# Kernel optimization log

Measured on AMD Instinct MI355X. Metric: run time of the kernel, lower is better.

The kernel has to match this reference:

```python
import jax, jax.numpy as jnp
import numpy as np
from jax import lax

B, T, BYTE_LEN, EMB = 8, 4096, 8, 64
FILTERS = [(1, 4), (2, 8), (3, 12), (4, 16), (5, 20), (6, 24), (7, 28)]
LAST_DIM = sum(c for _, c in FILTERS)  # 112
OUT_DIM = 512


def setup_inputs() -> dict:
    key = jax.random.key(0)
    ks = jax.random.split(key, 32)
    inp = {"features": jax.random.normal(ks[0], (B, T, BYTE_LEN, EMB), dtype=jnp.float32)}
    for i, (w, c) in enumerate(FILTERS):
        inp[f"conv_w{i+1}"] = jax.random.normal(ks[1 + i], (c, EMB, w), dtype=jnp.float32) * 0.05
        inp[f"conv_b{i+1}"] = jax.random.normal(ks[8 + i], (c,), dtype=jnp.float32) * 0.05
    inp["hw_w1"] = jax.random.normal(ks[15], (2 * LAST_DIM, LAST_DIM), dtype=jnp.float32) * 0.05
    inp["hw_b1"] = jnp.concatenate([jnp.zeros(LAST_DIM), jnp.ones(LAST_DIM)]).astype(jnp.float32)
    inp["hw_w2"] = jax.random.normal(ks[16], (2 * LAST_DIM, LAST_DIM), dtype=jnp.float32) * 0.05
    inp["hw_b2"] = jnp.concatenate([jnp.zeros(LAST_DIM), jnp.ones(LAST_DIM)]).astype(jnp.float32)
    inp["proj_w"] = jax.random.normal(ks[17], (OUT_DIM, LAST_DIM), dtype=jnp.float32) * 0.05
    inp["proj_b"] = jax.random.normal(ks[18], (OUT_DIM,), dtype=jnp.float32) * 0.05
    return inp


def _conv_branch(x, w, b):
    # x: [N, EMB, BYTE_LEN], w: [out_c, EMB, width] -> max over time, relu -> [N, out_c]
    y = lax.conv_general_dilated(x, w, window_strides=(1,), padding='VALID',
                                 dimension_numbers=('NCH', 'OIH', 'NCH'))
    y = y + b[None, :, None]
    return jax.nn.relu(jnp.max(y, axis=-1))


def _highway_layer(x, w, b):
    p = x @ w.T + b
    proj_x, gate = jnp.split(p, 2, axis=-1)
    g = jax.nn.sigmoid(gate)
    return g * x + (1.0 - g) * jax.nn.relu(proj_x)


def reference(features, conv_w1, conv_w2, conv_w3, conv_w4, conv_w5, conv_w6, conv_w7,
              conv_b1, conv_b2, conv_b3, conv_b4, conv_b5, conv_b6, conv_b7,
              hw_w1, hw_b1, hw_w2, hw_b2, proj_w, proj_b):
    b, t, byte_len, emb = features.shape
    # transpose(2,3).view(-1, emb, byte_len)
    x = features.transpose(0, 1, 3, 2).reshape(-1, emb, byte_len)  # [B*T, EMB, BYTE_LEN]
    ws = [conv_w1, conv_w2, conv_w3, conv_w4, conv_w5, conv_w6, conv_w7]
    bs = [conv_b1, conv_b2, conv_b3, conv_b4, conv_b5, conv_b6, conv_b7]
    branches = [_conv_branch(x, w, bb) for w, bb in zip(ws, bs)]
    h = jnp.concatenate(branches, axis=-1)  # [B*T, LAST_DIM]
    h = _highway_layer(h, hw_w1, hw_b1)
    h = _highway_layer(h, hw_w2, hw_b2)
    out = h @ proj_w.T + proj_b  # [B*T, OUT_DIM]
    return out.reshape(b, t, -1)
```

## Files before the change

kernel.cpp:

```cpp
#include <hip/hip_runtime.h>

typedef __attribute__((ext_vector_type(8))) short short8;
typedef __attribute__((ext_vector_type(4))) float f32x4;

#define NPOS 32768
#define KDIM 512
#define NCT  30
#define CHUNK_BYTES 30720

__device__ __forceinline__ unsigned short f2bf(float x) {
    unsigned u = __float_as_uint(x);
    return (unsigned short)((u + 0x7FFFu + ((u >> 16) & 1u)) >> 16);
}
__device__ __forceinline__ float bf2f(unsigned short h) {
    return __uint_as_float(((unsigned)h) << 16);
}

__device__ __forceinline__ void stage16(const void* g, void* l, int lane) {
    __builtin_amdgcn_global_load_lds(
        (const __attribute__((address_space(1))) unsigned int*)g,
        (__attribute__((address_space(3))) unsigned int*)l, 16, 0, 0);
}

__global__ void prep_kernel(const float* __restrict__ w1, const float* __restrict__ w2,
                            const float* __restrict__ w3, const float* __restrict__ w4,
                            const float* __restrict__ w5, const float* __restrict__ w6,
                            const float* __restrict__ w7, const float* __restrict__ hw1,
                            const float* __restrict__ hw2, const float* __restrict__ pw,
                            unsigned short* __restrict__ WC, unsigned short* __restrict__ W1s,
                            unsigned short* __restrict__ W2s, unsigned short* __restrict__ Ps) {
    int gid = blockIdx.x * 256 + threadIdx.x;
    if (gid < 245760) {
        int k = gid / 480, col = gid % 480;
        const float* wp; int cbnd, NP, C, W;
        if (col < 32)       { wp = w1; cbnd = 0;   NP = 8; C = 4;  W = 1; }
        else if (col < 96)  { wp = w2; cbnd = 32;  NP = 7; C = 8;  W = 2; }
        else if (col < 176) { wp = w3; cbnd = 96;  NP = 6; C = 12; W = 3; }
        else if (col < 256) { wp = w4; cbnd = 176; NP = 5; C = 16; W = 4; }
        else if (col < 336) { wp = w5; cbnd = 256; NP = 4; C = 20; W = 5; }
        else if (col < 416) { wp = w6; cbnd = 336; NP = 3; C = 24; W = 6; }
        else                { wp = w7; cbnd = 416; NP = 2; C = 28; W = 7; }
        int c2 = col - cbnd, oc = c2 / NP, p = c2 - oc * NP;
        int j = k >> 6, e = k & 63, dk = j - p;
        float v = 0.f;
        if (oc < C && dk >= 0 && dk < W) v = wp[(oc * 64 + e) * W + dk];
        int q = k >> 5, kr = k & 31;
        WC[((q * NCT + (col >> 4)) * 64 + ((kr >> 3) * 16 + (col & 15))) * 8 + (kr & 7)] = f2bf(v);
    } else if (gid < 245760 + 57344) {
        int x = gid - 245760;
        const float* src = (x < 28672) ? hw1 : hw2;
        unsigned short* dst = (x < 28672) ? W1s : W2s;
        if (x >= 28672) x -= 28672;
        int k = x / 224, n = x % 224;
        float v = (k < 112) ? src[n * 112 + k] : 0.f;
        int q = k >> 5, kr = k & 31;
        dst[((q * 14 + (n >> 4)) * 64 + ((kr >> 3) * 16 + (n & 15))) * 8 + (kr & 7)] = f2bf(v);
    } else if (gid < 245760 + 57344 + 65536) {
        int x = gid - 303104;
        int k = x / 512, n = x % 512;
        float v = (k < 112) ? pw[n * 112 + k] : 0.f;
        int q = k >> 5, kr = k & 31;
        Ps[((q * 32 + (n >> 4)) * 64 + ((kr >> 3) * 16 + (n & 15))) * 8 + (kr & 7)] = f2bf(v);
    }
}

template <int T0, int NT>
__device__ __forceinline__ void dump_phase(float* Cb, const f32x4* acc, int wave, int lane) {
    int r0 = wave * 16 + ((lane >> 4) * 4);
    int c0 = lane & 15;
#pragma unroll
    for (int tt = 0; tt < NT; ++tt)
#pragma unroll
        for (int r = 0; r < 4; ++r)
            Cb[(r0 + r) * 161 + tt * 16 + c0] = acc[T0 + tt][r];
}

__device__ void reduce_phase(const float* Cb, unsigned short* ht, int tid,
                             int cA, int NPA, int choffA, int colbA, const float* cbA,
                             int cB, int NPB, int choffB, int colbB, const float* cbB) {
    int noc = cA + cB;
    for (int idx = tid; idx < 64 * noc; idx += 256) {
        int row = idx & 63, ocp = idx >> 6;
        bool isB = ocp >= cA;
        int oc = isB ? ocp - cA : ocp;
        int NP = isB ? NPB : NPA;
        int colb = isB ? colbB : colbA;
        int choff = isB ? choffB : choffA;
        const float* cb = isB ? cbB : cbA;
        const float* src = Cb + row * 161 + colb + oc * NP;
        float m = src[0];
        for (int k = 1; k < NP; ++k) m = fmaxf(m, src[k]);
        float v = fmaxf(m + cb[oc], 0.f);
        ht[row * 128 + choff + oc] = f2bf(v);
    }
}

__global__ __launch_bounds__(256, 2) void conv_gemm(
        const float* __restrict__ feat, const unsigned short* __restrict__ WC,
        const float* cb0, const float* cb1, const float* cb2, const float* cb3,
        const float* cb4, const float* cb5, const float* cb6,
        unsigned short* __restrict__ hg) {
    __shared__ __align__(16) char sm[61440];
    const int tid = threadIdx.x, lane = tid & 63, wave = tid >> 6;
    const int c0 = lane & 15, kq = lane >> 4;
    const int m0 = blockIdx.x * 64;

    const float* arow = feat + (size_t)(m0 + wave * 16 + c0) * KDIM + kq * 8;
    short8 af[16];
#pragma unroll
    for (int q = 0; q < 16; ++q) {
        float t[8];
        *(float4*)(t)     = *(const float4*)(arow + q * 32);
        *(float4*)(t + 4) = *(const float4*)(arow + q * 32 + 4);
        short8 v;
#pragma unroll
        for (int i = 0; i < 8; ++i) v[i] = (short)f2bf(t[i]);
        af[q] = v;
    }

    f32x4 zero = {0.f, 0.f, 0.f, 0.f};
    f32x4 acc[NCT];
#pragma unroll
    for (int t = 0; t < NCT; ++t) acc[t] = zero;

    for (int i = tid; i < 1920; i += 256)
        stage16(WC + i * 8, sm + (i - lane) * 16, lane);

#pragma unroll
    for (int q = 0; q < 16; ++q) {
        __syncthreads();
        if (q < 15) {
            const unsigned short* src = WC + (q + 1) * (CHUNK_BYTES / 2);
            char* dst = sm + ((q + 1) & 1) * CHUNK_BYTES;
            for (int i = tid; i < 1920; i += 256)
                stage16(src + i * 8, dst + (i - lane) * 16, lane);
        }
        const char* bb = sm + (q & 1) * CHUNK_BYTES;
#pragma unroll
        for (int t = 0; t < NCT; ++t) {
            short8 b = *(const short8*)(bb + (t * 64 + lane) * 16);
            acc[t] = __builtin_amdgcn_mfma_f32_16x16x32_bf16(af[q], b, acc[t], 0, 0, 0);
        }
    }

    float* Cb = (float*)sm;
    unsigned short* ht = (unsigned short*)(sm + 41216);
    __syncthreads();
    for (int i = tid; i < 1024; i += 256)
        ht[(i >> 4) * 128 + 112 + (i & 15)] = 0;
    dump_phase<0, 6>(Cb, acc, wave, lane);
    __syncthreads();
    reduce_phase(Cb, ht, tid, 4, 8, 0, 0, cb0, 8, 7, 4, 32, cb1);
    __syncthreads();
    dump_phase<6, 10>(Cb, acc, wave, lane);
    __syncthreads();
    reduce_phase(Cb, ht, tid, 12, 6, 12, 0, cb2, 16, 5, 24, 80, cb3);
    __syncthreads();
    dump_phase<16, 10>(Cb, acc, wave, lane);
    __syncthreads();
    reduce_phase(Cb, ht, tid, 20, 4, 40, 0, cb4, 24, 3, 60, 80, cb5);
    __syncthreads();
    dump_phase<26, 4>(Cb, acc, wave, lane);
    __syncthreads();
    reduce_phase(Cb, ht, tid, 28, 2, 84, 0, cb6, 0, 1, 0, 0, cb6);
    __syncthreads();
    uint4* dst = (uint4*)(hg + (size_t)m0 * 128);
    for (int i = tid; i < 1024; i += 256) dst[i] = ((const uint4*)ht)[i];
}

__global__ __launch_bounds__(256, 2) void tail_kernel(
        const unsigned short* __restrict__ hg, const unsigned short* __restrict__ W1,
        const unsigned short* __restrict__ W2, const unsigned short* __restrict__ PW,
        const float* __restrict__ hb1, const float* __restrict__ hb2,
        const float* __restrict__ pb, float* __restrict__ out) {
    __shared__ __align__(16) char sm[65536];
    const int tid = threadIdx.x, lane = tid & 63, wave = tid >> 6;
    const int c0 = lane & 15, kq = lane >> 4;
    const int m0 = blockIdx.x * 64;
    f32x4 zero = {0.f, 0.f, 0.f, 0.f};

    short8 a2[4];
#pragma unroll
    for (int q = 0; q < 4; ++q)
        a2[q] = *(const short8*)(hg + (size_t)(m0 + wave * 16 + c0) * 128 + q * 32 + kq * 8);

    for (int i = tid; i < 3584; i += 256)
        stage16(W1 + i * 8, sm + (i - lane) * 16, lane);
    __syncthreads();
    f32x4 acc2[14];
#pragma unroll
    for (int t = 0; t < 14; ++t) acc2[t] = zero;
#pragma unroll
    for (int t = 0; t < 14; ++t)
#pragma unroll
        for (int q = 0; q < 4; ++q) {
            short8 b = *(const short8*)(sm + ((q * 14 + t) * 64 + lane) * 16);
            acc2[t] = __builtin_amdgcn_mfma_f32_16x16x32_bf16(a2[q], b, acc2[t], 0, 0, 0);
        }
    __syncthreads();

    unsigned short* ht = (unsigned short*)sm;
#pragma unroll
    for (int t = 0; t < 7; ++t) {
        float bp = hb1[t * 16 + c0], bg = hb1[112 + t * 16 + c0];
#pragma unroll
        for (int r = 0; r < 4; ++r) {
            int row = wave * 16 + kq * 4 + r;
            int col = t * 16 + c0;
            float px = acc2[t][r] + bp;
            float gt = acc2[t + 7][r] + bg;
            float g = 1.f / (1.f + __expf(-gt));
            float hres = bf2f(hg[(size_t)(m0 + row) * 128 + col]);
            ht[row * 136 + col] = f2bf(g * hres + (1.f - g) * fmaxf(px, 0.f));
        }
    }
    for (int z = lane; z < 256; z += 64)
        ht[(wave * 16 + (z >> 4)) * 136 + 112 + (z & 15)] = 0;

    short8 a3[4];
#pragma unroll
    for (int q = 0; q < 4; ++q)
        a3[q] = *(const short8*)((const char*)ht + (wave * 16 + c0) * 272 + q * 64 + kq * 16);

    char* wbuf = sm + 17408;
    f32x4 acc3[14];
#pragma unroll
    for (int t = 0; t < 14; ++t) acc3[t] = zero;
    for (int i = tid; i < 1792; i += 256)
        stage16(W2 + i * 8, wbuf + (i - lane) * 16, lane);
    __syncthreads();
#pragma unroll
    for (int t = 0; t < 14; ++t)
#pragma unroll
        for (int q = 0; q < 2; ++q) {
            short8 b = *(const short8*)(wbuf + ((q * 14 + t) * 64 + lane) * 16);
            acc3[t] = __builtin_amdgcn_mfma_f32_16x16x32_bf16(a3[q], b, acc3[t], 0, 0, 0);
        }
    __syncthreads();
    for (int i = tid; i < 1792; i += 256)
        stage16(W2 + 14336 + i * 8, wbuf + (i - lane) * 16, lane);
    __syncthreads();
#pragma unroll
    for (int t = 0; t < 14; ++t)
#pragma unroll
        for (int q = 0; q < 2; ++q) {
            short8 b = *(const short8*)(wbuf + ((q * 14 + t) * 64 + lane) * 16);
            acc3[t] = __builtin_amdgcn_mfma_f32_16x16x32_bf16(a3[2 + q], b, acc3[t], 0, 0, 0);
        }

#pragma unroll
    for (int t = 0; t < 7; ++t) {
        float bp = hb2[t * 16 + c0], bg = hb2[112 + t * 16 + c0];
#pragma unroll
        for (int r = 0; r < 4; ++r) {
            int row = wave * 16 + kq * 4 + r;
            int col = t * 16 + c0;
            float px = acc3[t][r] + bp;
            float gt = acc3[t + 7][r] + bg;
            float g = 1.f / (1.f + __expf(-gt));
            float hres = bf2f(ht[row * 136 + col]);
            ht[row * 136 + col] = f2bf(g * hres + (1.f - g) * fmaxf(px, 0.f));
        }
    }

    short8 a4[4];
#pragma unroll
    for (int q = 0; q < 4; ++q)
        a4[q] = *(const short8*)((const char*)ht + (wave * 16 + c0) * 272 + q * 64 + kq * 16);

    f32x4 acc4[32];
#pragma unroll
    for (int t = 0; t < 32; ++t) acc4[t] = zero;
#pragma unroll
    for (int q = 0; q < 4; ++q) {
        __syncthreads();
        for (int i = tid; i < 2048; i += 256)
            stage16(PW + q * 16384 + i * 8, wbuf + (i - lane) * 16, lane);
        __syncthreads();
#pragma unroll
        for (int t = 0; t < 32; ++t) {
            short8 b = *(const short8*)(wbuf + (t * 64 + lane) * 16);
            acc4[t] = __builtin_amdgcn_mfma_f32_16x16x32_bf16(a4[q], b, acc4[t], 0, 0, 0);
        }
    }

    float* ot = (float*)sm;
#pragma unroll
    for (int half = 0; half < 2; ++half) {
        __syncthreads();
#pragma unroll
        for (int t16 = 0; t16 < 16; ++t16) {
            int col = (half * 16 + t16) * 16 + c0;
            float b = pb[col];
#pragma unroll
            for (int r = 0; r < 4; ++r)
                ot[(wave * 16 + kq * 4 + r) * 256 + t16 * 16 + c0] = acc4[half * 16 + t16][r] + b;
        }
        __syncthreads();
        for (int i = tid; i < 4096; i += 256) {
            int row = i >> 6, c = i & 63;
            *(float4*)(out + (size_t)(m0 + row) * 512 + half * 256 + c * 4) = ((const float4*)ot)[i];
        }
    }
}

extern "C" void kernel_launch(void* const* d_in, const int* in_sizes, int n_in,
                              void* d_out, int out_size, void* d_ws, size_t ws_size,
                              hipStream_t stream) {
    const float* feat = (const float*)d_in[0];
    const float* cw[7];
    const float* cb[7];
    for (int f = 0; f < 7; ++f) {
        cw[f] = (const float*)d_in[1 + 2 * f];
        cb[f] = (const float*)d_in[2 + 2 * f];
    }
    const float* hw_w1 = (const float*)d_in[15];
    const float* hw_b1 = (const float*)d_in[16];
    const float* hw_w2 = (const float*)d_in[17];
    const float* hw_b2 = (const float*)d_in[18];
    const float* pw    = (const float*)d_in[19];
    const float* pb    = (const float*)d_in[20];
    float* out = (float*)d_out;

    char* ws = (char*)d_ws;
    unsigned short* WC  = (unsigned short*)ws;
    unsigned short* W1s = (unsigned short*)(ws + 491520);
    unsigned short* W2s = (unsigned short*)(ws + 548864);
    unsigned short* Ps  = (unsigned short*)(ws + 606208);
    unsigned short* hg  = (unsigned short*)(ws + 737280);

    prep_kernel<<<1440, 256, 0, stream>>>(cw[0], cw[1], cw[2], cw[3], cw[4], cw[5], cw[6],
                                          hw_w1, hw_w2, pw, WC, W1s, W2s, Ps);
    conv_gemm<<<512, 256, 0, stream>>>(feat, WC, cb[0], cb[1], cb[2], cb[3], cb[4], cb[5], cb[6], hg);
    tail_kernel<<<512, 256, 0, stream>>>(hg, W1s, W2s, Ps, hw_b1, hw_b2, pb, out);
}
```

Before: 202.0 us.

## Fuse conv GEMM with highway/projection tail and reshape conv wave tiling

Merges the conv GEMM and tail kernels into one kernel, so the intermediate h tile stays in shared memory instead of making a round trip through global memory. The conv GEMM is re-tiled so each wave covers all 64 rows and a slice of about 8 column tiles, and the conv weight layout is changed to match. Feature loads are pipelined one k-chunk ahead with bf16 conversion per step, and W1 staging is split in half to fit shared memory. This removes one launch and the hg traffic, but adds register pressure (a 4x8 accumulator array) and leaves waves with uneven work.

```diff
diff --git a/kernel.cpp b/kernel.cpp
--- a/kernel.cpp
+++ b/kernel.cpp
@@ -3,10 +3,7 @@
 typedef __attribute__((ext_vector_type(8))) short short8;
 typedef __attribute__((ext_vector_type(4))) float f32x4;
 
-#define NPOS 32768
 #define KDIM 512
-#define NCT  30
-#define CHUNK_BYTES 30720
 
 __device__ __forceinline__ unsigned short f2bf(float x) {
     unsigned u = __float_as_uint(x);
@@ -44,8 +41,7 @@
         int j = k >> 6, e = k & 63, dk = j - p;
         float v = 0.f;
         if (oc < C && dk >= 0 && dk < W) v = wp[(oc * 64 + e) * W + dk];
-        int q = k >> 5, kr = k & 31;
-        WC[((q * NCT + (col >> 4)) * 64 + ((kr >> 3) * 16 + (col & 15))) * 8 + (kr & 7)] = f2bf(v);
+        WC[((k >> 4) * 30 + (col >> 4)) * 256 + ((k >> 3) & 1) * 128 + (col & 15) * 8 + (k & 7)] = f2bf(v);
     } else if (gid < 245760 + 57344) {
         int x = gid - 245760;
         const float* src = (x < 28672) ? hw1 : hw2;
@@ -64,15 +60,20 @@
     }
 }
 
-template <int T0, int NT>
-__device__ __forceinline__ void dump_phase(float* Cb, const f32x4* acc, int wave, int lane) {
-    int r0 = wave * 16 + ((lane >> 4) * 4);
-    int c0 = lane & 15;
-#pragma unroll
-    for (int tt = 0; tt < NT; ++tt)
-#pragma unroll
-        for (int r = 0; r < 4; ++r)
-            Cb[(r0 + r) * 161 + tt * 16 + c0] = acc[T0 + tt][r];
+template <int T0, int T1>
+__device__ __forceinline__ void dump_conv(float* Cb, const f32x4 (&acc)[4][8],
+                                          int tbase, int ntile, int kq, int c0) {
+#pragma unroll
+    for (int j = 0; j < 8; ++j) {
+        int t = tbase + j;
+        if (j < ntile && t >= T0 && t < T1) {
+#pragma unroll
+            for (int rf = 0; rf < 4; ++rf)
+#pragma unroll
+                for (int r = 0; r < 4; ++r)
+                    Cb[(rf * 16 + kq * 4 + r) * 161 + (t - T0) * 16 + c0] = acc[rf][j][r];
+        }
+    }
 }
 
 __device__ void reduce_phase(const float* Cb, unsigned short* ht, int tid,
@@ -91,115 +92,136 @@
         float m = src[0];
         for (int k = 1; k < NP; ++k) m = fmaxf(m, src[k]);
         float v = fmaxf(m + cb[oc], 0.f);
-        ht[row * 128 + choff + oc] = f2bf(v);
-    }
-}
-
-__global__ __launch_bounds__(256, 2) void conv_gemm(
+        ht[row * 136 + choff + oc] = f2bf(v);
+    }
+}
+
+__global__ __launch_bounds__(256, 2) void fused_kernel(
         const float* __restrict__ feat, const unsigned short* __restrict__ WC,
         const float* cb0, const float* cb1, const float* cb2, const float* cb3,
         const float* cb4, const float* cb5, const float* cb6,
-        unsigned short* __restrict__ hg) {
-    __shared__ __align__(16) char sm[61440];
-    const int tid = threadIdx.x, lane = tid & 63, wave = tid >> 6;
-    const int c0 = lane & 15, kq = lane >> 4;
-    const int m0 = blockIdx.x * 64;
-
-    const float* arow = feat + (size_t)(m0 + wave * 16 + c0) * KDIM + kq * 8;
-    short8 af[16];
-#pragma unroll
-    for (int q = 0; q < 16; ++q) {
-        float t[8];
-        *(float4*)(t)     = *(const float4*)(arow + q * 32);
-        *(float4*)(t + 4) = *(const float4*)(arow + q * 32 + 4);
-        short8 v;
-#pragma unroll
-        for (int i = 0; i < 8; ++i) v[i] = (short)f2bf(t[i]);
-        af[q] = v;
-    }
-
-    f32x4 zero = {0.f, 0.f, 0.f, 0.f};
-    f32x4 acc[NCT];
-#pragma unroll
-    for (int t = 0; t < NCT; ++t) acc[t] = zero;
-
-    for (int i = tid; i < 1920; i += 256)
-        stage16(WC + i * 8, sm + (i - lane) * 16, lane);
-
-#pragma unroll
-    for (int q = 0; q < 16; ++q) {
-        __syncthreads();
-        if (q < 15) {
-            const unsigned short* src = WC + (q + 1) * (CHUNK_BYTES / 2);
-            char* dst = sm + ((q + 1) & 1) * CHUNK_BYTES;
-            for (int i = tid; i < 1920; i += 256)
-                stage16(src + i * 8, dst + (i - lane) * 16, lane);
-        }
-        const char* bb = sm + (q & 1) * CHUNK_BYTES;
-#pragma unroll
-        for (int t = 0; t < NCT; ++t) {
-            short8 b = *(const short8*)(bb + (t * 64 + lane) * 16);
-            acc[t] = __builtin_amdgcn_mfma_f32_16x16x32_bf16(af[q], b, acc[t], 0, 0, 0);
-        }
-    }
-
-    float* Cb = (float*)sm;
-    unsigned short* ht = (unsigned short*)(sm + 41216);
-    __syncthreads();
-    for (int i = tid; i < 1024; i += 256)
-        ht[(i >> 4) * 128 + 112 + (i & 15)] = 0;
-    dump_phase<0, 6>(Cb, acc, wave, lane);
-    __syncthreads();
-    reduce_phase(Cb, ht, tid, 4, 8, 0, 0, cb0, 8, 7, 4, 32, cb1);
-    __syncthreads();
-    dump_phase<6, 10>(Cb, acc, wave, lane);
-    __syncthreads();
-    reduce_phase(Cb, ht, tid, 12, 6, 12, 0, cb2, 16, 5, 24, 80, cb3);
-    __syncthreads();
-    dump_phase<16, 10>(Cb, acc, wave, lane);
-    __syncthreads();
-    reduce_phase(Cb, ht, tid, 20, 4, 40, 0, cb4, 24, 3, 60, 80, cb5);
-    __syncthreads();
-    dump_phase<26, 4>(Cb, acc, wave, lane);
-    __syncthreads();
-    reduce_phase(Cb, ht, tid, 28, 2, 84, 0, cb6, 0, 1, 0, 0, cb6);
-    __syncthreads();
-    uint4* dst = (uint4*)(hg + (size_t)m0 * 128);
-    for (int i = tid; i < 1024; i += 256) dst[i] = ((const uint4*)ht)[i];
-}
-
-__global__ __launch_bounds__(256, 2) void tail_kernel(
-        const unsigned short* __restrict__ hg, const unsigned short* __restrict__ W1,
-        const unsigned short* __restrict__ W2, const unsigned short* __restrict__ PW,
+        const unsigned short* __restrict__ W1, const unsigned short* __restrict__ W2,
+        const unsigned short* __restrict__ PW,
         const float* __restrict__ hb1, const float* __restrict__ hb2,
         const float* __restrict__ pb, float* __restrict__ out) {
     __shared__ __align__(16) char sm[65536];
     const int tid = threadIdx.x, lane = tid & 63, wave = tid >> 6;
     const int c0 = lane & 15, kq = lane >> 4;
     const int m0 = blockIdx.x * 64;
+    const int tbase = wave * 8 - (wave == 3 ? 1 : 0);
+    const int ntile = (wave < 2) ? 8 : 7;
     f32x4 zero = {0.f, 0.f, 0.f, 0.f};
 
+    f32x4 acc[4][8];
+#pragma unroll
+    for (int rf = 0; rf < 4; ++rf)
+#pragma unroll
+        for (int j = 0; j < 8; ++j) acc[rf][j] = zero;
+
+    for (int i = tid; i < 1920; i += 256)
+        stage16(WC + i * 8, sm + (i - lane) * 16, lane);
+    const float* fb = feat + (size_t)(m0 + c0) * KDIM + kq * 8;
+    float4 ap[4][2];
+#pragma unroll
+    for (int rf = 0; rf < 4; ++rf) {
+        ap[rf][0] = *(const float4*)(fb + rf * 16 * KDIM);
+        ap[rf][1] = *(const float4*)(fb + rf * 16 * KDIM + 4);
+    }
+    const int bofs = (kq >> 1) * 15360 + (kq & 1) * 256 + c0 * 16;
+
+#pragma unroll
+    for (int q = 0; q < 16; ++q) {
+        __syncthreads();
+        if (q < 15) {
+            const unsigned short* src = WC + (q + 1) * 15360;
+            char* dst = sm + ((q + 1) & 1) * 30720;
+            for (int i = tid; i < 1920; i += 256)
+                stage16(src + i * 8, dst + (i - lane) * 16, lane);
+        }
+        short8 aq[4];
+#pragma unroll
+        for (int rf = 0; rf < 4; ++rf) {
+            float t[8];
+            *(float4*)t = ap[rf][0]; *(float4*)(t + 4) = ap[rf][1];
+            short8 v;
+#pragma unroll
+            for (int i = 0; i < 8; ++i) v[i] = (short)f2bf(t[i]);
+            aq[rf] = v;
+        }
+        if (q < 15) {
+#pragma unroll
+            for (int rf = 0; rf < 4; ++rf) {
+                ap[rf][0] = *(const float4*)(fb + rf * 16 * KDIM + (q + 1) * 32);
+                ap[rf][1] = *(const float4*)(fb + rf * 16 * KDIM + (q + 1) * 32 + 4);
+            }
+        }
+        const char* bb = sm + (q & 1) * 30720;
+#pragma unroll
+        for (int j = 0; j < 8; ++j) {
+            if (j < ntile) {
+                short8 b = *(const short8*)(bb + bofs + (tbase + j) * 512);
+#pragma unroll
+                for (int rf = 0; rf < 4; ++rf)
+                    acc[rf][j] = __builtin_amdgcn_mfma_f32_16x16x32_bf16(aq[rf], b, acc[rf][j], 0, 0, 0);
+            }
+        }
+    }
+
+    float* Cb = (float*)(sm + 17408);
+    unsigned short* ht = (unsigned short*)sm;
+    __syncthreads();
+    for (int i = tid; i < 1024; i += 256)
+        ht[(i >> 4) * 136 + 112 + (i & 15)] = 0;
+    dump_conv<0, 6>(Cb, acc, tbase, ntile, kq, c0);
+    __syncthreads();
+    reduce_phase(Cb, ht, tid, 4, 8, 0, 0, cb0, 8, 7, 4, 32, cb1);
+    __syncthreads();
+    dump_conv<6, 16>(Cb, acc, tbase, ntile, kq, c0);
+    __syncthreads();
+    reduce_phase(Cb, ht, tid, 12, 6, 12, 0, cb2, 16, 5, 24, 80, cb3);
+    __syncthreads();
+    dump_conv<16, 26>(Cb, acc, tbase, ntile, kq, c0);
+    __syncthreads();
+    reduce_phase(Cb, ht, tid, 20, 4, 40, 0, cb4, 24, 3, 60, 80, cb5);
+    __syncthreads();
+    dump_conv<26, 30>(Cb, acc, tbase, ntile, kq, c0);
+    __syncthreads();
+    reduce_phase(Cb, ht, tid, 28, 2, 84, 0, cb6, 0, 1, 0, 0, cb6);
+    __syncthreads();
+
+    char* wbuf = sm + 17408;
+
     short8 a2[4];
 #pragma unroll
     for (int q = 0; q < 4; ++q)
-        a2[q] = *(const short8*)(hg + (size_t)(m0 + wave * 16 + c0) * 128 + q * 32 + kq * 8);
-
-    for (int i = tid; i < 3584; i += 256)
-        stage16(W1 + i * 8, sm + (i - lane) * 16, lane);
-    __syncthreads();
+        a2[q] = *(const short8*)((const char*)ht + (wave * 16 + c0) * 272 + q * 64 + kq * 16);
+
     f32x4 acc2[14];
 #pragma unroll
     for (int t = 0; t < 14; ++t) acc2[t] = zero;
+    __syncthreads();
+    for (int i = tid; i < 1792; i += 256)
+        stage16(W1 + i * 8, wbuf + (i - lane) * 16, lane);
+    __syncthreads();
 #pragma unroll
     for (int t = 0; t < 14; ++t)
 #pragma unroll
-        for (int q = 0; q < 4; ++q) {
-            short8 b = *(const short8*)(sm + ((q * 14 + t) * 64 + lane) * 16);
+        for (int q = 0; q < 2; ++q) {
+            short8 b = *(const short8*)(wbuf + ((q * 14 + t) * 64 + lane) * 16);
             acc2[t] = __builtin_amdgcn_mfma_f32_16x16x32_bf16(a2[q], b, acc2[t], 0, 0, 0);
         }
     __syncthreads();
-
-    unsigned short* ht = (unsigned short*)sm;
+    for (int i = tid; i < 1792; i += 256)
+        stage16(W1 + 14336 + i * 8, wbuf + (i - lane) * 16, lane);
+    __syncthreads();
+#pragma unroll
+    for (int t = 0; t < 14; ++t)
+#pragma unroll
+        for (int q = 0; q < 2; ++q) {
+            short8 b = *(const short8*)(wbuf + ((q * 14 + t) * 64 + lane) * 16);
+            acc2[t] = __builtin_amdgcn_mfma_f32_16x16x32_bf16(a2[2 + q], b, acc2[t], 0, 0, 0);
+        }
+
 #pragma unroll
     for (int t = 0; t < 7; ++t) {
         float bp = hb1[t * 16 + c0], bg = hb1[112 + t * 16 + c0];
@@ -210,22 +232,20 @@
             float px = acc2[t][r] + bp;
             float gt = acc2[t + 7][r] + bg;
             float g = 1.f / (1.f + __expf(-gt));
-            float hres = bf2f(hg[(size_t)(m0 + row) * 128 + col]);
+            float hres = bf2f(ht[row * 136 + col]);
             ht[row * 136 + col] = f2bf(g * hres + (1.f - g) * fmaxf(px, 0.f));
         }
     }
-    for (int z = lane; z < 256; z += 64)
-        ht[(wave * 16 + (z >> 4)) * 136 + 112 + (z & 15)] = 0;
 
     short8 a3[4];
 #pragma unroll
     for (int q = 0; q < 4; ++q)
         a3[q] = *(const short8*)((const char*)ht + (wave * 16 + c0) * 272 + q * 64 + kq * 16);
 
-    char* wbuf = sm + 17408;
     f32x4 acc3[14];
 #pragma unroll
     for (int t = 0; t < 14; ++t) acc3[t] = zero;
+    __syncthreads();
     for (int i = tid; i < 1792; i += 256)
         stage16(W2 + i * 8, wbuf + (i - lane) * 16, lane);
     __syncthreads();
@@ -327,10 +347,10 @@
     unsigned short* W1s = (unsigned short*)(ws + 491520);
     unsigned short* W2s = (unsigned short*)(ws + 548864);
     unsigned short* Ps  = (unsigned short*)(ws + 606208);
-    unsigned short* hg  = (unsigned short*)(ws + 737280);
 
     prep_kernel<<<1440, 256, 0, stream>>>(cw[0], cw[1], cw[2], cw[3], cw[4], cw[5], cw[6],
                                           hw_w1, hw_w2, pw, WC, W1s, W2s, Ps);
-    conv_gemm<<<512, 256, 0, stream>>>(feat, WC, cb[0], cb[1], cb[2], cb[3], cb[4], cb[5], cb[6], hg);
-    tail_kernel<<<512, 256, 0, stream>>>(hg, W1s, W2s, Ps, hw_b1, hw_b2, pb, out);
-}
+    fused_kernel<<<512, 256, 0, stream>>>(feat, WC,
+                                          cb[0], cb[1], cb[2], cb[3], cb[4], cb[5], cb[6],
+                                          W1s, W2s, Ps, hw_b1, hw_b2, pb, out);
+}
```

Result: no change. 204.8 us (+1.4%).
